# Optimization experiments

Hardware: AMD Instinct MI355X
Metric: run time of the kernel (lower is better)

The kernel has to match this reference:

```python
import jax, jax.numpy as jnp
import numpy as np

K_SIZE = 7
D_MODEL = 128
D_Q = 64
N_HEADS = 4
D_FF = 512
EPS = 1e-5


def _windows(x, k):
    # x: [N,E,H,W] -> [N,E,P,H,W]; zero-padded local k x k windows,
    # row-major over (dy,dx), matching nn.Unfold ordering.
    p = k // 2
    N, E, H, W = x.shape
    xp = jnp.pad(x, ((0, 0), (0, 0), (p, p), (p, p)))
    ws = [xp[:, :, i:i + H, j:j + W] for i in range(k) for j in range(k)]
    return jnp.stack(ws, axis=2)


def _layernorm(x, g, b):
    m = jnp.mean(x, -1, keepdims=True)
    v = jnp.var(x, -1, keepdims=True)
    return (x - m) * jax.lax.rsqrt(v + EPS) * g + b


def setup_inputs() -> dict:
    key = jax.random.key(0)
    ks = jax.random.split(key, 12)
    E, Q, F = D_MODEL, D_Q, D_FF

    def g(k, shape, s=0.02):
        return jax.random.normal(k, shape, jnp.float32) * s

    return dict(
        x=jax.random.normal(ks[0], (4, E, 64, 64), jnp.float32),
        qcoeff=jax.random.normal(ks[1], (4, Q), jnp.float32),
        wq=g(ks[2], (E, E)), bq=jnp.zeros((E,), jnp.float32),
        wk=g(ks[3], (E, E)), bk=jnp.zeros((E,), jnp.float32),
        wv=g(ks[4], (E, E)), bv=jnp.zeros((E,), jnp.float32),
        rel_bias=jnp.zeros((N_HEADS, K_SIZE * K_SIZE), jnp.float32),
        ln1_g=jnp.ones((E,), jnp.float32), ln1_b=jnp.zeros((E,), jnp.float32),
        bil_w=g(ks[5], (E, E, Q)), bil_b=jnp.zeros((E,), jnp.float32),
        ln2_g=jnp.ones((E,), jnp.float32), ln2_b=jnp.zeros((E,), jnp.float32),
        w1=g(ks[6], (F, E)), b1=jnp.zeros((F,), jnp.float32),
        w2=g(ks[7], (E, F)), b2=jnp.zeros((E,), jnp.float32),
    )


def reference(x, qcoeff, wq, bq, wk, bk, wv, bv, rel_bias, ln1_g, ln1_b,
              bil_w, bil_b, ln2_g, ln2_b, w1, b1, w2, b2):
    N, E, H, W = x.shape
    Nh = N_HEADS
    Hd = E // Nh
    P = K_SIZE * K_SIZE

    x_nhwc = jnp.transpose(x, (0, 2, 3, 1))              # [N,H,W,E]
    xn = _layernorm(x_nhwc, ln1_g, ln1_b)
    xnc = jnp.transpose(xn, (0, 3, 1, 2))                # [N,E,H,W]

    # 1x1-conv projections
    q = jnp.einsum('nchw,oc->nohw', xnc, wq) + bq[None, :, None, None]
    k = jnp.einsum('nchw,oc->nohw', xnc, wk) + bk[None, :, None, None]
    v = jnp.einsum('nchw,oc->nohw', xnc, wv) + bv[None, :, None, None]

    # local windows of K/V: [N,Nh,Hd,P,H,W]
    Kw = _windows(k, K_SIZE).reshape(N, Nh, Hd, P, H, W)
    Vw = _windows(v, K_SIZE).reshape(N, Nh, Hd, P, H, W)
    Qh = q.reshape(N, Nh, Hd, H, W)

    scores = jnp.einsum('nhdyx,nhdpyx->nhpyx', Qh, Kw)
    scores = scores + rel_bias[None, :, :, None, None]
    attn = jax.nn.softmax(scores, axis=2)                # softmax over P
    out = jnp.einsum('nhpyx,nhdpyx->nhdyx', attn, Vw).reshape(N, E, H, W)
    z0 = jnp.transpose(out, (0, 2, 3, 1))                # [N,H,W,E]

    # Bilinear(z0, qcoeff): qcoeff constant per (H,W) -> contract once per batch
    t = jnp.einsum('oiq,nq->noi', bil_w, qcoeff)         # [N,E,E]
    z1 = jnp.einsum('nhwi,noi->nhwo', z0, t) + bil_b

    z2 = z1 + x_nhwc
    z3 = _layernorm(z2, ln2_g, ln2_b)
    h1 = jax.nn.gelu(z3 @ w1.T + b1, approximate=False)  # dropout inactive (eval)
    z4 = h1 @ w2.T + b2 + z2
    return jnp.transpose(z4, (0, 3, 1, 2))               # [N,E,H,W]
```

## Files before the change

kernel.cpp:

```cpp
#include <hip/hip_runtime.h>
#include <cmath>

#define EPS 1e-5f
#define SZ 2097152

typedef __attribute__((ext_vector_type(8))) short short8;
typedef __attribute__((ext_vector_type(4))) float floatx4;

__device__ __forceinline__ float dot4(float4 a, float4 b) {
  return fmaf(a.x, b.x, fmaf(a.y, b.y, fmaf(a.z, b.z, a.w * b.w)));
}

__device__ __forceinline__ short f2bf(float f) {
  union { float f; unsigned u; } v; v.f = f;
  unsigned r = v.u + 0x7fff + ((v.u >> 16) & 1);
  return (short)(r >> 16);
}

#define MFMA16(a, b, c) __builtin_amdgcn_mfma_f32_16x16x32_bf16(a, b, c, 0, 0, 0)

__global__ __launch_bounds__(256) void k_prep(const float* __restrict__ w1,
    const float* __restrict__ w2, const float* __restrict__ wq,
    const float* __restrict__ wk, const float* __restrict__ wv,
    const float* __restrict__ bil_w, const float* __restrict__ qcoeff,
    short* __restrict__ w1bf, short* __restrict__ w2bf,
    short* __restrict__ wqbf, short* __restrict__ wkbf, short* __restrict__ wvbf,
    short* __restrict__ tb) {
  __shared__ float qs[256];
  int tid = threadIdx.x;
  qs[tid] = qcoeff[tid];
  __syncthreads();
  int tid0 = blockIdx.x * 256 + tid;
  int stride = gridDim.x * 256;
  for (int i = tid0; i < 16384; i += stride) {
    int flat = i * 4; int f = flat >> 7, c = flat & 127;
    float4 v = *(const float4*)&w1[flat];
    short t4[4] = {f2bf(v.x), f2bf(v.y), f2bf(v.z), f2bf(v.w)};
    *(uint2*)&w1bf[f * 136 + c] = *(uint2*)t4;
  }
  for (int i = tid0; i < 16384; i += stride) {
    int flat = i * 4; int o = flat >> 9, j = flat & 511;
    int ck = j >> 7, jj = j & 127;
    float4 v = *(const float4*)&w2[flat];
    short t4[4] = {f2bf(v.x), f2bf(v.y), f2bf(v.z), f2bf(v.w)};
    *(uint2*)&w2bf[(ck * 128 + o) * 136 + jj] = *(uint2*)t4;
  }
  for (int i = tid0; i < 4096; i += stride) {
    int flat = i * 4; int o = flat >> 7, c = flat & 127;
    float4 a = *(const float4*)&wq[flat];
    float4 b = *(const float4*)&wk[flat];
    float4 cc = *(const float4*)&wv[flat];
    short ta[4] = {f2bf(a.x), f2bf(a.y), f2bf(a.z), f2bf(a.w)};
    short tb4[4] = {f2bf(b.x), f2bf(b.y), f2bf(b.z), f2bf(b.w)};
    short tc[4] = {f2bf(cc.x), f2bf(cc.y), f2bf(cc.z), f2bf(cc.w)};
    *(uint2*)&wqbf[o * 136 + c] = *(uint2*)ta;
    *(uint2*)&wkbf[o * 136 + c] = *(uint2*)tb4;
    *(uint2*)&wvbf[o * 136 + c] = *(uint2*)tc;
  }
  {
    int flat = tid0;
    const float* wrow = bil_w + (size_t)flat * 64;
    float acc[4] = {0.f, 0.f, 0.f, 0.f};
    for (int qq = 0; qq < 64; qq += 4) {
      float4 w4 = *(const float4*)&wrow[qq];
#pragma unroll
      for (int nn = 0; nn < 4; ++nn) {
        const float* qc = &qs[nn * 64 + qq];
        acc[nn] = fmaf(w4.x, qc[0], fmaf(w4.y, qc[1], fmaf(w4.z, qc[2], fmaf(w4.w, qc[3], acc[nn]))));
      }
    }
    int o = flat >> 7, i = flat & 127;
#pragma unroll
    for (int nn = 0; nn < 4; ++nn) tb[nn * 17408 + o * 136 + i] = f2bf(acc[nn]);
  }
}

__global__ __launch_bounds__(1024) void k_qkvln(const float* __restrict__ x,
    const float* __restrict__ g, const float* __restrict__ b,
    const short* __restrict__ wqbf, const short* __restrict__ wkbf,
    const short* __restrict__ wvbf, const float* __restrict__ bq,
    const float* __restrict__ bk, const float* __restrict__ bv,
    float* __restrict__ xnhwc, short* __restrict__ qbf,
    short* __restrict__ kbf, short* __restrict__ vtb) {
  __shared__ float tile[128 * 65];
  __shared__ float mres[64], rres[64];
  __shared__ __align__(16) short xs[64 * 136];
  __shared__ __align__(16) short ws[128 * 136];
  int tid = threadIdx.x;
  int bid = blockIdx.x;
  int n = bid >> 6, y = bid & 63;
  const float* xb = x + (size_t)n * (128 * 4096) + y * 64;
  for (int it = 0; it < 8; ++it) {
    int flat = it * 1024 + tid;
    int c = flat >> 6, xp = flat & 63;
    tile[c * 65 + xp] = xb[(size_t)c * 4096 + xp];
  }
  __syncthreads();
  {
    int px = tid >> 4, cl = tid & 15;
    float s = 0.f, sq = 0.f;
#pragma unroll
    for (int j = 0; j < 8; ++j) {
      float v = tile[(cl * 8 + j) * 65 + px];
      s += v; sq += v * v;
    }
    s += __shfl_xor(s, 1);  sq += __shfl_xor(sq, 1);
    s += __shfl_xor(s, 2);  sq += __shfl_xor(sq, 2);
    s += __shfl_xor(s, 4);  sq += __shfl_xor(sq, 4);
    s += __shfl_xor(s, 8);  sq += __shfl_xor(sq, 8);
    if (cl == 0) {
      float m = s * (1.f / 128.f);
      float var = sq * (1.f / 128.f) - m * m;
      mres[px] = m;
      rres[px] = rsqrtf(var + EPS);
    }
  }
  __syncthreads();
  size_t rowbase = (size_t)bid * 8192;
  for (int it = 0; it < 8; ++it) {
    int flat = it * 1024 + tid;
    int c = flat & 127, px = flat >> 7;
    float v = tile[c * 65 + px];
    xnhwc[rowbase + flat] = v;
    xs[px * 136 + c] = f2bf((v - mres[px]) * rres[px] * g[c] + b[c]);
  }
  __syncthreads();
  int w = tid >> 6, lane = tid & 63;
  int quad = lane >> 4, r16 = lane & 15;
  int wm = w & 3, wn = w >> 2;
  int strip = wm * 16;
  short8 a[4];
#pragma unroll
  for (int kk = 0; kk < 4; ++kk)
    a[kk] = *(const short8*)&xs[(strip + r16) * 136 + kk * 32 + quad * 8];
  const short* wptr[3] = {wqbf, wkbf, wvbf};
  const float* bptr[3] = {bq, bk, bv};
  for (int m = 0; m < 3; ++m) {
    __syncthreads();
    const short* wp = wptr[m];
    for (int i = tid; i < 2176; i += 1024)
      *(short8*)&ws[i * 8] = *(const short8*)&wp[i * 8];
    __syncthreads();
    const float* bb = bptr[m];
#pragma unroll
    for (int nt = 0; nt < 2; ++nt) {
      int o0 = wn * 32 + nt * 16;
      floatx4 acc = {0.f, 0.f, 0.f, 0.f};
#pragma unroll
      for (int kk = 0; kk < 4; ++kk) {
        short8 bfr = *(const short8*)&ws[(o0 + r16) * 136 + kk * 32 + quad * 8];
        acc = MFMA16(a[kk], bfr, acc);
      }
      float bv2 = bb[o0 + r16];
      if (m < 2) {
        short* dst = (m == 0) ? qbf : kbf;
#pragma unroll
        for (int r = 0; r < 4; ++r) {
          int px = strip + quad * 4 + r;
          dst[rowbase + px * 128 + o0 + r16] = f2bf(acc[r] + bv2);
        }
      } else {
        short t4[4] = {f2bf(acc[0] + bv2), f2bf(acc[1] + bv2),
                       f2bf(acc[2] + bv2), f2bf(acc[3] + bv2)};
        *(uint2*)&vtb[(size_t)(n * 128 + o0 + r16) * 4096 + y * 64 + strip + quad * 4] =
            *(uint2*)t4;
      }
    }
  }
}

__global__ __launch_bounds__(1024) void k_at(const short* __restrict__ qbf,
    const short* __restrict__ kbf, const short* __restrict__ vtb,
    const float* __restrict__ rel_bias, const short* __restrict__ tb,
    const float* __restrict__ bil_b, const float* __restrict__ xnhwc,
    const float* __restrict__ g2, const float* __restrict__ b2ln,
    const short* __restrict__ w1bf, const float* __restrict__ b1,
    const short* __restrict__ w2bf, const float* __restrict__ b2,
    float* __restrict__ out) {
  __shared__ __align__(16) char smem[140544];
  short* z3s = (short*)(smem + 89344);
  float* z2s = (float*)(smem + 106752);
  int tid = threadIdx.x;
  int bid = blockIdx.x;
  int n = bid >> 6, y = bid & 63;
  int w16 = tid >> 6, lane = tid & 63;
  int quad = lane >> 4, r16 = lane & 15;
  {
    int h = w16 >> 2, sw = w16 & 3;
    int strip = sw * 16;
    float* ssfw = (float*)(smem + w16 * 3200);
    short* Abw = (short*)(smem + 51200 + w16 * 2176);
    float* biasw = (float*)(smem + 86016 + w16 * 208);
    {
      unsigned* ad = (unsigned*)Abw;
      for (int i = lane; i < 544; i += 64) ad[i] = 0u;
    }
    if (lane < 49) biasw[lane] = rel_bias[h * 49 + lane];
    const short* qrow = qbf + (size_t)n * 524288 + (size_t)y * 8192 + h * 32;
    short8 qf = *(const short8*)&qrow[(strip + r16) * 128 + quad * 8];
    const short* kbp = kbf + (size_t)n * 524288 + h * 32;
#pragma unroll
    for (int r = 0; r < 7; ++r) {
      int yy = y + r - 3;
      bool yok = (unsigned)yy < 64u;
      int yyc = min(max(yy, 0), 63);
#pragma unroll
      for (int t = 0; t < 2; ++t) {
        int xxc = (sw + t) * 16 + r16;
        int gx = xxc - 3;
        bool ok = yok && ((unsigned)gx < 64u);
        int gxc = min(max(gx, 0), 63);
        short8 bf = *(const short8*)&kbp[(size_t)(yyc * 64 + gxc) * 128 + quad * 8];
        floatx4 c = MFMA16(qf, bf, ((floatx4){0.f, 0.f, 0.f, 0.f}));
#pragma unroll
        for (int rr = 0; rr < 4; ++rr) {
          int lrow = quad * 4 + rr;
          int dx = xxc - (strip + lrow);
          if ((unsigned)dx < 7u) {
            float val = ok ? c[rr] : 0.f;
            ssfw[lrow * 50 + r * 7 + dx] = val + biasw[r * 7 + dx];
          }
        }
      }
    }
    {
      int lrow = lane >> 2, sub = lane & 3;
      int p0 = sub * 12, cnt = (sub == 3) ? 13 : 12;
      float sv[13];
      float mx = -1e30f;
      for (int pi = 0; pi < cnt; ++pi) { sv[pi] = ssfw[lrow * 50 + p0 + pi]; mx = fmaxf(mx, sv[pi]); }
      mx = fmaxf(mx, __shfl_xor(mx, 1));
      mx = fmaxf(mx, __shfl_xor(mx, 2));
      float sum = 0.f;
      for (int pi = 0; pi < cnt; ++pi) { float e = __expf(sv[pi] - mx); sv[pi] = e; sum += e; }
      sum += __shfl_xor(sum, 1);
      sum += __shfl_xor(sum, 2);
      float inv = 1.f / sum;
      for (int pi = 0; pi < cnt; ++pi) ssfw[lrow * 50 + p0 + pi] = sv[pi] * inv;
    }
    floatx4 oacc[2] = {(floatx4){0.f, 0.f, 0.f, 0.f}, (floatx4){0.f, 0.f, 0.f, 0.f}};
    int kk0 = (sw == 3) ? 1 : 0;
    int kk1 = (sw == 0) ? 0 : 1;
    int lrow = lane >> 2, sub = lane & 3;
    int pxg = strip + lrow;
    const short* vbp = vtb + (size_t)(n * 128 + h * 32) * 4096;
    for (int r = 0; r < 7; ++r) {
      int yy = y + r - 3;
      bool yok = (unsigned)yy < 64u;
      int yyc = min(max(yy, 0), 63);
      int c0 = pxg + sub - 3;
      if ((unsigned)c0 < 64u) Abw[lrow * 68 + c0] = f2bf(ssfw[lrow * 50 + r * 7 + sub]);
      int c1 = pxg + sub + 1;
      if (sub < 3 && (unsigned)c1 < 64u)
        Abw[lrow * 68 + c1] = f2bf(ssfw[lrow * 50 + r * 7 + sub + 4]);
      for (int kk = kk0; kk <= kk1; ++kk) {
        short8 af = *(const short8*)&Abw[r16 * 68 + kk * 32 + quad * 8];
#pragma unroll
        for (int nt = 0; nt < 2; ++nt) {
          short8 vf = *(const short8*)&vbp[(size_t)(nt * 16 + r16) * 4096 + yyc * 64 + kk * 32 + quad * 8];
          if (!yok) vf = (short8){0, 0, 0, 0, 0, 0, 0, 0};
          oacc[nt] = MFMA16(af, vf, oacc[nt]);
        }
      }
    }
#pragma unroll
    for (int nt = 0; nt < 2; ++nt)
#pragma unroll
      for (int rr = 0; rr < 4; ++rr) {
        int px = strip + quad * 4 + rr;
        z3s[px * 136 + h * 32 + nt * 16 + r16] = f2bf(oacc[nt][rr]);
      }
  }
  __syncthreads();
  short* R1s = (short*)smem;
  short* w2c = (short*)(smem + 34816);
  short* h1s = (short*)(smem + 69632);
  float* outt = (float*)smem;
  size_t rowbase = (size_t)bid * 8192;
  const short* tn = tb + (size_t)n * 17408;
  for (int i = tid; i < 2176; i += 1024)
    *(short8*)&R1s[i * 8] = *(const short8*)&tn[i * 8];
  __syncthreads();
  int wm = w16 & 3, wn = w16 >> 2;
  int strip = wm * 16;
  {
    short8 a[4];
#pragma unroll
    for (int kk = 0; kk < 4; ++kk)
      a[kk] = *(const short8*)&z3s[(strip + r16) * 136 + kk * 32 + quad * 8];
#pragma unroll
    for (int nt = 0; nt < 2; ++nt) {
      int o0 = wn * 32 + nt * 16;
      floatx4 acc = {0.f, 0.f, 0.f, 0.f};
#pragma unroll
      for (int kk = 0; kk < 4; ++kk) {
        short8 bfr = *(const short8*)&R1s[(o0 + r16) * 136 + kk * 32 + quad * 8];
        acc = MFMA16(a[kk], bfr, acc);
      }
      float bb = bil_b[o0 + r16];
#pragma unroll
      for (int r = 0; r < 4; ++r) {
        int px = strip + quad * 4 + r;
        z2s[px * 132 + o0 + r16] = acc[r] + bb + xnhwc[rowbase + px * 128 + o0 + r16];
      }
    }
  }
  __syncthreads();
  {
    int px = tid >> 4, cl = tid & 15;
    float4 v0 = *(const float4*)&z2s[px * 132 + cl * 8];
    float4 v1 = *(const float4*)&z2s[px * 132 + cl * 8 + 4];
    float s = v0.x + v0.y + v0.z + v0.w + v1.x + v1.y + v1.z + v1.w;
    float sq = dot4(v0, v0) + dot4(v1, v1);
    s += __shfl_xor(s, 1);  sq += __shfl_xor(sq, 1);
    s += __shfl_xor(s, 2);  sq += __shfl_xor(sq, 2);
    s += __shfl_xor(s, 4);  sq += __shfl_xor(sq, 4);
    s += __shfl_xor(s, 8);  sq += __shfl_xor(sq, 8);
    float m = s * (1.f / 128.f);
    float var = sq * (1.f / 128.f) - m * m;
    float rr = rsqrtf(var + EPS);
    int c0 = cl * 8;
    short t8[8];
#pragma unroll
    for (int j = 0; j < 8; ++j) {
      float vv = (j < 4) ? (&v0.x)[j] : (&v1.x)[j - 4];
      t8[j] = f2bf((vv - m) * rr * g2[c0 + j] + b2ln[c0 + j]);
    }
    *(uint4*)&z3s[px * 136 + c0] = *(uint4*)t8;
  }
  __syncthreads();
  short8 a3[4];
#pragma unroll
  for (int kk = 0; kk < 4; ++kk)
    a3[kk] = *(const short8*)&z3s[(strip + r16) * 136 + kk * 32 + quad * 8];
  floatx4 zacc[2];
  zacc[0] = (floatx4){0.f, 0.f, 0.f, 0.f};
  zacc[1] = (floatx4){0.f, 0.f, 0.f, 0.f};
  for (int fc = 0; fc < 512; fc += 128) {
    __syncthreads();
    const short* w1src = w1bf + fc * 136;
    const short* w2src = w2bf + (fc >> 7) * 17408;
    for (int i = tid; i < 2176; i += 1024) {
      *(short8*)&R1s[i * 8] = *(const short8*)&w1src[i * 8];
      *(short8*)&w2c[i * 8] = *(const short8*)&w2src[i * 8];
    }
    __syncthreads();
#pragma unroll
    for (int nt = 0; nt < 2; ++nt) {
      int f0 = wn * 32 + nt * 16;
      floatx4 acc = {0.f, 0.f, 0.f, 0.f};
#pragma unroll
      for (int kk = 0; kk < 4; ++kk) {
        short8 bfr = *(const short8*)&R1s[(f0 + r16) * 136 + kk * 32 + quad * 8];
        acc = MFMA16(a3[kk], bfr, acc);
      }
      float bb1 = b1[fc + f0 + r16];
#pragma unroll
      for (int r = 0; r < 4; ++r) {
        float hv = acc[r] + bb1;
        float ge = 0.5f * hv * (1.f + erff(hv * 0.70710678118f));
        h1s[(strip + quad * 4 + r) * 136 + f0 + r16] = f2bf(ge);
      }
    }
    __syncthreads();
    short8 ah[4];
#pragma unroll
    for (int kk = 0; kk < 4; ++kk)
      ah[kk] = *(const short8*)&h1s[(strip + r16) * 136 + kk * 32 + quad * 8];
#pragma unroll
    for (int nt = 0; nt < 2; ++nt) {
      int o0 = wn * 32 + nt * 16;
#pragma unroll
      for (int kk = 0; kk < 4; ++kk) {
        short8 bfr = *(const short8*)&w2c[(o0 + r16) * 136 + kk * 32 + quad * 8];
        zacc[nt] = MFMA16(ah[kk], bfr, zacc[nt]);
      }
    }
  }
  __syncthreads();
#pragma unroll
  for (int nt = 0; nt < 2; ++nt) {
    int o0 = wn * 32 + nt * 16;
    float bb = b2[o0 + r16];
#pragma unroll
    for (int r = 0; r < 4; ++r) {
      int px = strip + quad * 4 + r;
      outt[(o0 + r16) * 65 + px] = zacc[nt][r] + bb + z2s[px * 132 + o0 + r16];
    }
  }
  __syncthreads();
  for (int it = 0; it < 8; ++it) {
    int flat = it * 1024 + tid;
    int o = flat >> 6, px = flat & 63;
    out[(((size_t)(n * 128 + o)) * 64 + y) * 64 + px] = outt[o * 65 + px];
  }
}

extern "C" void kernel_launch(void* const* d_in, const int* in_sizes, int n_in,
                              void* d_out, int out_size, void* d_ws, size_t ws_size,
                              hipStream_t stream) {
  const float* x        = (const float*)d_in[0];
  const float* qcoeff   = (const float*)d_in[1];
  const float* wq       = (const float*)d_in[2];
  const float* bq       = (const float*)d_in[3];
  const float* wk       = (const float*)d_in[4];
  const float* bk       = (const float*)d_in[5];
  const float* wv       = (const float*)d_in[6];
  const float* bv       = (const float*)d_in[7];
  const float* rel_bias = (const float*)d_in[8];
  const float* ln1_g    = (const float*)d_in[9];
  const float* ln1_b    = (const float*)d_in[10];
  const float* bil_w    = (const float*)d_in[11];
  const float* bil_b    = (const float*)d_in[12];
  const float* ln2_g    = (const float*)d_in[13];
  const float* ln2_b    = (const float*)d_in[14];
  const float* w1       = (const float*)d_in[15];
  const float* b1       = (const float*)d_in[16];
  const float* w2       = (const float*)d_in[17];
  const float* b2       = (const float*)d_in[18];
  float* out = (float*)d_out;

  float* ws = (float*)d_ws;
  float* x_nhwc = ws;
  short* qbf = (short*)(ws + 2 * SZ);
  short* kbf = qbf + SZ;
  short* vtb = kbf + SZ;
  short* bf     = (short*)(ws + 4 * SZ);
  short* tb     = bf;
  short* w1bf   = bf + 4 * 17408;
  short* w2bf   = w1bf + 512 * 136;
  short* wqbf   = w2bf + 4 * 17408;
  short* wkbf   = wqbf + 17408;
  short* wvbf   = wkbf + 17408;

  k_prep<<<64, 256, 0, stream>>>(w1, w2, wq, wk, wv, bil_w, qcoeff,
                                 w1bf, w2bf, wqbf, wkbf, wvbf, tb);
  k_qkvln<<<256, 1024, 0, stream>>>(x, ln1_g, ln1_b, wqbf, wkbf, wvbf,
                                    bq, bk, bv, x_nhwc, qbf, kbf, vtb);
  k_at<<<256, 1024, 0, stream>>>(qbf, kbf, vtb, rel_bias, tb, bil_b, x_nhwc,
                                 ln2_g, ln2_b, w1bf, b1, w2bf, b2, out);
}
```

Measured before the change: 149.8 us.

## Fuse prep, QKV/LN and attention kernels into one cooperative kernel

Merges the three separate kernels (weight conversion, LayerNorm plus QKV projection, attention plus MLP) into a single cooperative launch that separates the phases with grid-wide syncs. The goal is to remove two kernel launch gaps and the tail idle time between kernels. The prep phase now runs on 256 blocks of 1024 threads instead of 64 blocks of 256. The cost is grid-sync overhead, and it requires all 256 blocks of 1024 threads with about 137KB of shared memory each to be co-resident on the device.

```diff
diff --git a/kernel.cpp b/kernel.cpp
--- a/kernel.cpp
+++ b/kernel.cpp
@@ -1,5 +1,8 @@
 #include <hip/hip_runtime.h>
+#include <hip/hip_cooperative_groups.h>
 #include <cmath>
+
+namespace cg = cooperative_groups;
 
 #define EPS 1e-5f
 #define SZ 2097152
@@ -19,170 +22,162 @@
 
 #define MFMA16(a, b, c) __builtin_amdgcn_mfma_f32_16x16x32_bf16(a, b, c, 0, 0, 0)
 
-__global__ __launch_bounds__(256) void k_prep(const float* __restrict__ w1,
-    const float* __restrict__ w2, const float* __restrict__ wq,
-    const float* __restrict__ wk, const float* __restrict__ wv,
-    const float* __restrict__ bil_w, const float* __restrict__ qcoeff,
-    short* __restrict__ w1bf, short* __restrict__ w2bf,
-    short* __restrict__ wqbf, short* __restrict__ wkbf, short* __restrict__ wvbf,
-    short* __restrict__ tb) {
-  __shared__ float qs[256];
-  int tid = threadIdx.x;
-  qs[tid] = qcoeff[tid];
-  __syncthreads();
-  int tid0 = blockIdx.x * 256 + tid;
-  int stride = gridDim.x * 256;
-  for (int i = tid0; i < 16384; i += stride) {
-    int flat = i * 4; int f = flat >> 7, c = flat & 127;
-    float4 v = *(const float4*)&w1[flat];
-    short t4[4] = {f2bf(v.x), f2bf(v.y), f2bf(v.z), f2bf(v.w)};
-    *(uint2*)&w1bf[f * 136 + c] = *(uint2*)t4;
-  }
-  for (int i = tid0; i < 16384; i += stride) {
-    int flat = i * 4; int o = flat >> 9, j = flat & 511;
-    int ck = j >> 7, jj = j & 127;
-    float4 v = *(const float4*)&w2[flat];
-    short t4[4] = {f2bf(v.x), f2bf(v.y), f2bf(v.z), f2bf(v.w)};
-    *(uint2*)&w2bf[(ck * 128 + o) * 136 + jj] = *(uint2*)t4;
-  }
-  for (int i = tid0; i < 4096; i += stride) {
-    int flat = i * 4; int o = flat >> 7, c = flat & 127;
-    float4 a = *(const float4*)&wq[flat];
-    float4 b = *(const float4*)&wk[flat];
-    float4 cc = *(const float4*)&wv[flat];
-    short ta[4] = {f2bf(a.x), f2bf(a.y), f2bf(a.z), f2bf(a.w)};
-    short tb4[4] = {f2bf(b.x), f2bf(b.y), f2bf(b.z), f2bf(b.w)};
-    short tc[4] = {f2bf(cc.x), f2bf(cc.y), f2bf(cc.z), f2bf(cc.w)};
-    *(uint2*)&wqbf[o * 136 + c] = *(uint2*)ta;
-    *(uint2*)&wkbf[o * 136 + c] = *(uint2*)tb4;
-    *(uint2*)&wvbf[o * 136 + c] = *(uint2*)tc;
-  }
-  {
-    int flat = tid0;
-    const float* wrow = bil_w + (size_t)flat * 64;
-    float acc[4] = {0.f, 0.f, 0.f, 0.f};
-    for (int qq = 0; qq < 64; qq += 4) {
-      float4 w4 = *(const float4*)&wrow[qq];
-#pragma unroll
-      for (int nn = 0; nn < 4; ++nn) {
-        const float* qc = &qs[nn * 64 + qq];
-        acc[nn] = fmaf(w4.x, qc[0], fmaf(w4.y, qc[1], fmaf(w4.z, qc[2], fmaf(w4.w, qc[3], acc[nn]))));
-      }
-    }
-    int o = flat >> 7, i = flat & 127;
-#pragma unroll
-    for (int nn = 0; nn < 4; ++nn) tb[nn * 17408 + o * 136 + i] = f2bf(acc[nn]);
-  }
-}
-
-__global__ __launch_bounds__(1024) void k_qkvln(const float* __restrict__ x,
-    const float* __restrict__ g, const float* __restrict__ b,
-    const short* __restrict__ wqbf, const short* __restrict__ wkbf,
-    const short* __restrict__ wvbf, const float* __restrict__ bq,
-    const float* __restrict__ bk, const float* __restrict__ bv,
-    float* __restrict__ xnhwc, short* __restrict__ qbf,
-    short* __restrict__ kbf, short* __restrict__ vtb) {
-  __shared__ float tile[128 * 65];
-  __shared__ float mres[64], rres[64];
-  __shared__ __align__(16) short xs[64 * 136];
-  __shared__ __align__(16) short ws[128 * 136];
+struct KParams {
+  const float *x, *qcoeff, *wq, *bq, *wk, *bk, *wv, *bv, *rel_bias;
+  const float *ln1_g, *ln1_b, *bil_w, *bil_b, *ln2_g, *ln2_b, *w1, *b1, *w2, *b2;
+  float* out;
+  float* x_nhwc;
+  short *qbf, *kbf, *vtb;
+  short *tb, *w1bf, *w2bf, *wqbf, *wkbf, *wvbf;
+};
+
+__global__ __launch_bounds__(1024) void k_all(KParams p) {
+  __shared__ __align__(16) char smem[140544];
+  cg::grid_group grid = cg::this_grid();
   int tid = threadIdx.x;
   int bid = blockIdx.x;
   int n = bid >> 6, y = bid & 63;
-  const float* xb = x + (size_t)n * (128 * 4096) + y * 64;
-  for (int it = 0; it < 8; ++it) {
-    int flat = it * 1024 + tid;
-    int c = flat >> 6, xp = flat & 63;
-    tile[c * 65 + xp] = xb[(size_t)c * 4096 + xp];
-  }
-  __syncthreads();
+
   {
-    int px = tid >> 4, cl = tid & 15;
-    float s = 0.f, sq = 0.f;
-#pragma unroll
-    for (int j = 0; j < 8; ++j) {
-      float v = tile[(cl * 8 + j) * 65 + px];
-      s += v; sq += v * v;
-    }
-    s += __shfl_xor(s, 1);  sq += __shfl_xor(sq, 1);
-    s += __shfl_xor(s, 2);  sq += __shfl_xor(sq, 2);
-    s += __shfl_xor(s, 4);  sq += __shfl_xor(sq, 4);
-    s += __shfl_xor(s, 8);  sq += __shfl_xor(sq, 8);
-    if (cl == 0) {
-      float m = s * (1.f / 128.f);
-      float var = sq * (1.f / 128.f) - m * m;
-      mres[px] = m;
-      rres[px] = rsqrtf(var + EPS);
-    }
-  }
-  __syncthreads();
-  size_t rowbase = (size_t)bid * 8192;
-  for (int it = 0; it < 8; ++it) {
-    int flat = it * 1024 + tid;
-    int c = flat & 127, px = flat >> 7;
-    float v = tile[c * 65 + px];
-    xnhwc[rowbase + flat] = v;
-    xs[px * 136 + c] = f2bf((v - mres[px]) * rres[px] * g[c] + b[c]);
-  }
-  __syncthreads();
-  int w = tid >> 6, lane = tid & 63;
-  int quad = lane >> 4, r16 = lane & 15;
-  int wm = w & 3, wn = w >> 2;
-  int strip = wm * 16;
-  short8 a[4];
-#pragma unroll
-  for (int kk = 0; kk < 4; ++kk)
-    a[kk] = *(const short8*)&xs[(strip + r16) * 136 + kk * 32 + quad * 8];
-  const short* wptr[3] = {wqbf, wkbf, wvbf};
-  const float* bptr[3] = {bq, bk, bv};
-  for (int m = 0; m < 3; ++m) {
-    __syncthreads();
-    const short* wp = wptr[m];
-    for (int i = tid; i < 2176; i += 1024)
-      *(short8*)&ws[i * 8] = *(const short8*)&wp[i * 8];
-    __syncthreads();
-    const float* bb = bptr[m];
-#pragma unroll
-    for (int nt = 0; nt < 2; ++nt) {
-      int o0 = wn * 32 + nt * 16;
-      floatx4 acc = {0.f, 0.f, 0.f, 0.f};
-#pragma unroll
-      for (int kk = 0; kk < 4; ++kk) {
-        short8 bfr = *(const short8*)&ws[(o0 + r16) * 136 + kk * 32 + quad * 8];
-        acc = MFMA16(a[kk], bfr, acc);
-      }
-      float bv2 = bb[o0 + r16];
-      if (m < 2) {
-        short* dst = (m == 0) ? qbf : kbf;
-#pragma unroll
-        for (int r = 0; r < 4; ++r) {
-          int px = strip + quad * 4 + r;
-          dst[rowbase + px * 128 + o0 + r16] = f2bf(acc[r] + bv2);
+    float* qs = (float*)smem;
+    if (tid < 256) qs[tid] = p.qcoeff[tid];
+    __syncthreads();
+    int gtid = bid * 1024 + tid;
+    if (gtid < 16384) {
+      int flat = gtid * 4;
+      {
+        int f = flat >> 7, c = flat & 127;
+        float4 v = *(const float4*)&p.w1[flat];
+        short t4[4] = {f2bf(v.x), f2bf(v.y), f2bf(v.z), f2bf(v.w)};
+        *(uint2*)&p.w1bf[f * 136 + c] = *(uint2*)t4;
+      }
+      {
+        int o = flat >> 9, j = flat & 511;
+        int ck = j >> 7, jj = j & 127;
+        float4 v = *(const float4*)&p.w2[flat];
+        short t4[4] = {f2bf(v.x), f2bf(v.y), f2bf(v.z), f2bf(v.w)};
+        *(uint2*)&p.w2bf[(ck * 128 + o) * 136 + jj] = *(uint2*)t4;
+      }
+      {
+        const float* wrow = p.bil_w + (size_t)gtid * 64;
+        float acc[4] = {0.f, 0.f, 0.f, 0.f};
+        for (int qq = 0; qq < 64; qq += 4) {
+          float4 w4 = *(const float4*)&wrow[qq];
+#pragma unroll
+          for (int nn = 0; nn < 4; ++nn) {
+            const float* qc = &qs[nn * 64 + qq];
+            acc[nn] = fmaf(w4.x, qc[0], fmaf(w4.y, qc[1], fmaf(w4.z, qc[2], fmaf(w4.w, qc[3], acc[nn]))));
+          }
         }
-      } else {
-        short t4[4] = {f2bf(acc[0] + bv2), f2bf(acc[1] + bv2),
-                       f2bf(acc[2] + bv2), f2bf(acc[3] + bv2)};
-        *(uint2*)&vtb[(size_t)(n * 128 + o0 + r16) * 4096 + y * 64 + strip + quad * 4] =
-            *(uint2*)t4;
-      }
-    }
-  }
-}
-
-__global__ __launch_bounds__(1024) void k_at(const short* __restrict__ qbf,
-    const short* __restrict__ kbf, const short* __restrict__ vtb,
-    const float* __restrict__ rel_bias, const short* __restrict__ tb,
-    const float* __restrict__ bil_b, const float* __restrict__ xnhwc,
-    const float* __restrict__ g2, const float* __restrict__ b2ln,
-    const short* __restrict__ w1bf, const float* __restrict__ b1,
-    const short* __restrict__ w2bf, const float* __restrict__ b2,
-    float* __restrict__ out) {
-  __shared__ __align__(16) char smem[140544];
+        int o = gtid >> 7, i = gtid & 127;
+#pragma unroll
+        for (int nn = 0; nn < 4; ++nn) p.tb[nn * 17408 + o * 136 + i] = f2bf(acc[nn]);
+      }
+    }
+    if (gtid < 4096) {
+      int flat = gtid * 4; int o = flat >> 7, c = flat & 127;
+      float4 a = *(const float4*)&p.wq[flat];
+      float4 b = *(const float4*)&p.wk[flat];
+      float4 cc = *(const float4*)&p.wv[flat];
+      short ta[4] = {f2bf(a.x), f2bf(a.y), f2bf(a.z), f2bf(a.w)};
+      short tb4[4] = {f2bf(b.x), f2bf(b.y), f2bf(b.z), f2bf(b.w)};
+      short tc[4] = {f2bf(cc.x), f2bf(cc.y), f2bf(cc.z), f2bf(cc.w)};
+      *(uint2*)&p.wqbf[o * 136 + c] = *(uint2*)ta;
+      *(uint2*)&p.wkbf[o * 136 + c] = *(uint2*)tb4;
+      *(uint2*)&p.wvbf[o * 136 + c] = *(uint2*)tc;
+    }
+  }
+  grid.sync();
+
+  {
+    float* tile = (float*)smem;
+    float* mres = (float*)(smem + 33280);
+    float* rres = (float*)(smem + 33536);
+    short* xs = (short*)(smem + 34048);
+    short* ws = (short*)(smem + 51456);
+    const float* xb = p.x + (size_t)n * (128 * 4096) + y * 64;
+    for (int it = 0; it < 8; ++it) {
+      int flat = it * 1024 + tid;
+      int c = flat >> 6, xp = flat & 63;
+      tile[c * 65 + xp] = xb[(size_t)c * 4096 + xp];
+    }
+    __syncthreads();
+    {
+      int px = tid >> 4, cl = tid & 15;
+      float s = 0.f, sq = 0.f;
+#pragma unroll
+      for (int j = 0; j < 8; ++j) {
+        float v = tile[(cl * 8 + j) * 65 + px];
+        s += v; sq += v * v;
+      }
+      s += __shfl_xor(s, 1);  sq += __shfl_xor(sq, 1);
+      s += __shfl_xor(s, 2);  sq += __shfl_xor(sq, 2);
+      s += __shfl_xor(s, 4);  sq += __shfl_xor(sq, 4);
+      s += __shfl_xor(s, 8);  sq += __shfl_xor(sq, 8);
+      if (cl == 0) {
+        float m = s * (1.f / 128.f);
+        float var = sq * (1.f / 128.f) - m * m;
+        mres[px] = m;
+        rres[px] = rsqrtf(var + EPS);
+      }
+    }
+    __syncthreads();
+    size_t rowbase = (size_t)bid * 8192;
+    for (int it = 0; it < 8; ++it) {
+      int flat = it * 1024 + tid;
+      int c = flat & 127, px = flat >> 7;
+      float v = tile[c * 65 + px];
+      p.x_nhwc[rowbase + flat] = v;
+      xs[px * 136 + c] = f2bf((v - mres[px]) * rres[px] * p.ln1_g[c] + p.ln1_b[c]);
+    }
+    __syncthreads();
+    int w = tid >> 6, lane = tid & 63;
+    int quad = lane >> 4, r16 = lane & 15;
+    int wm = w & 3, wn = w >> 2;
+    int strip = wm * 16;
+    short8 a[4];
+#pragma unroll
+    for (int kk = 0; kk < 4; ++kk)
+      a[kk] = *(const short8*)&xs[(strip + r16) * 136 + kk * 32 + quad * 8];
+    const short* wptr[3] = {p.wqbf, p.wkbf, p.wvbf};
+    const float* bptr[3] = {p.bq, p.bk, p.bv};
+    for (int m = 0; m < 3; ++m) {
+      __syncthreads();
+      const short* wp = wptr[m];
+      for (int i = tid; i < 2176; i += 1024)
+        *(short8*)&ws[i * 8] = *(const short8*)&wp[i * 8];
+      __syncthreads();
+      const float* bb = bptr[m];
+#pragma unroll
+      for (int nt = 0; nt < 2; ++nt) {
+        int o0 = wn * 32 + nt * 16;
+        floatx4 acc = {0.f, 0.f, 0.f, 0.f};
+#pragma unroll
+        for (int kk = 0; kk < 4; ++kk) {
+          short8 bfr = *(const short8*)&ws[(o0 + r16) * 136 + kk * 32 + quad * 8];
+          acc = MFMA16(a[kk], bfr, acc);
+        }
+        float bv2 = bb[o0 + r16];
+        if (m < 2) {
+          short* dst = (m == 0) ? p.qbf : p.kbf;
+#pragma unroll
+          for (int r = 0; r < 4; ++r) {
+            int px = strip + quad * 4 + r;
+            dst[rowbase + px * 128 + o0 + r16] = f2bf(acc[r] + bv2);
+          }
+        } else {
+          short t4[4] = {f2bf(acc[0] + bv2), f2bf(acc[1] + bv2),
+                         f2bf(acc[2] + bv2), f2bf(acc[3] + bv2)};
+          *(uint2*)&p.vtb[(size_t)(n * 128 + o0 + r16) * 4096 + y * 64 + strip + quad * 4] =
+              *(uint2*)t4;
+        }
+      }
+    }
+  }
+  grid.sync();
+
   short* z3s = (short*)(smem + 89344);
   float* z2s = (float*)(smem + 106752);
-  int tid = threadIdx.x;
-  int bid = blockIdx.x;
-  int n = bid >> 6, y = bid & 63;
   int w16 = tid >> 6, lane = tid & 63;
   int quad = lane >> 4, r16 = lane & 15;
   {
@@ -195,10 +190,10 @@
       unsigned* ad = (unsigned*)Abw;
       for (int i = lane; i < 544; i += 64) ad[i] = 0u;
     }
-    if (lane < 49) biasw[lane] = rel_bias[h * 49 + lane];
-    const short* qrow = qbf + (size_t)n * 524288 + (size_t)y * 8192 + h * 32;
+    if (lane < 49) biasw[lane] = p.rel_bias[h * 49 + lane];
+    const short* qrow = p.qbf + (size_t)n * 524288 + (size_t)y * 8192 + h * 32;
     short8 qf = *(const short8*)&qrow[(strip + r16) * 128 + quad * 8];
-    const short* kbp = kbf + (size_t)n * 524288 + h * 32;
+    const short* kbp = p.kbf + (size_t)n * 524288 + h * 32;
 #pragma unroll
     for (int r = 0; r < 7; ++r) {
       int yy = y + r - 3;
@@ -243,7 +238,7 @@
     int kk1 = (sw == 0) ? 0 : 1;
     int lrow = lane >> 2, sub = lane & 3;
     int pxg = strip + lrow;
-    const short* vbp = vtb + (size_t)(n * 128 + h * 32) * 4096;
+    const short* vbp = p.vtb + (size_t)(n * 128 + h * 32) * 4096;
     for (int r = 0; r < 7; ++r) {
       int yy = y + r - 3;
       bool yok = (unsigned)yy < 64u;
@@ -277,7 +272,7 @@
   short* h1s = (short*)(smem + 69632);
   float* outt = (float*)smem;
   size_t rowbase = (size_t)bid * 8192;
-  const short* tn = tb + (size_t)n * 17408;
+  const short* tn = p.tb + (size_t)n * 17408;
   for (int i = tid; i < 2176; i += 1024)
     *(short8*)&R1s[i * 8] = *(const short8*)&tn[i * 8];
   __syncthreads();
@@ -297,11 +292,11 @@
         short8 bfr = *(const short8*)&R1s[(o0 + r16) * 136 + kk * 32 + quad * 8];
         acc = MFMA16(a[kk], bfr, acc);
       }
-      float bb = bil_b[o0 + r16];
+      float bb = p.bil_b[o0 + r16];
 #pragma unroll
       for (int r = 0; r < 4; ++r) {
         int px = strip + quad * 4 + r;
-        z2s[px * 132 + o0 + r16] = acc[r] + bb + xnhwc[rowbase + px * 128 + o0 + r16];
+        z2s[px * 132 + o0 + r16] = acc[r] + bb + p.x_nhwc[rowbase + px * 128 + o0 + r16];
       }
     }
   }
@@ -324,7 +319,7 @@
 #pragma unroll
     for (int j = 0; j < 8; ++j) {
       float vv = (j < 4) ? (&v0.x)[j] : (&v1.x)[j - 4];
-      t8[j] = f2bf((vv - m) * rr * g2[c0 + j] + b2ln[c0 + j]);
+      t8[j] = f2bf((vv - m) * rr * p.ln2_g[c0 + j] + p.ln2_b[c0 + j]);
     }
     *(uint4*)&z3s[px * 136 + c0] = *(uint4*)t8;
   }
@@ -338,8 +333,8 @@
   zacc[1] = (floatx4){0.f, 0.f, 0.f, 0.f};
   for (int fc = 0; fc < 512; fc += 128) {
     __syncthreads();
-    const short* w1src = w1bf + fc * 136;
-    const short* w2src = w2bf + (fc >> 7) * 17408;
+    const short* w1src = p.w1bf + fc * 136;
+    const short* w2src = p.w2bf + (fc >> 7) * 17408;
     for (int i = tid; i < 2176; i += 1024) {
       *(short8*)&R1s[i * 8] = *(const short8*)&w1src[i * 8];
       *(short8*)&w2c[i * 8] = *(const short8*)&w2src[i * 8];
@@ -354,7 +349,7 @@
         short8 bfr = *(const short8*)&R1s[(f0 + r16) * 136 + kk * 32 + quad * 8];
         acc = MFMA16(a3[kk], bfr, acc);
       }
-      float bb1 = b1[fc + f0 + r16];
+      float bb1 = p.b1[fc + f0 + r16];
 #pragma unroll
       for (int r = 0; r < 4; ++r) {
         float hv = acc[r] + bb1;
@@ -381,7 +376,7 @@
 #pragma unroll
   for (int nt = 0; nt < 2; ++nt) {
     int o0 = wn * 32 + nt * 16;
-    float bb = b2[o0 + r16];
+    float bb = p.b2[o0 + r16];
 #pragma unroll
     for (int r = 0; r < 4; ++r) {
       int px = strip + quad * 4 + r;
@@ -392,51 +387,48 @@
   for (int it = 0; it < 8; ++it) {
     int flat = it * 1024 + tid;
     int o = flat >> 6, px = flat & 63;
-    out[(((size_t)(n * 128 + o)) * 64 + y) * 64 + px] = outt[o * 65 + px];
+    p.out[(((size_t)(n * 128 + o)) * 64 + y) * 64 + px] = outt[o * 65 + px];
   }
 }
 
 extern "C" void kernel_launch(void* const* d_in, const int* in_sizes, int n_in,
                               void* d_out, int out_size, void* d_ws, size_t ws_size,
                               hipStream_t stream) {
-  const float* x        = (const float*)d_in[0];
-  const float* qcoeff   = (const float*)d_in[1];
-  const float* wq       = (const float*)d_in[2];
-  const float* bq       = (const float*)d_in[3];
-  const float* wk       = (const float*)d_in[4];
-  const float* bk       = (const float*)d_in[5];
-  const float* wv       = (const float*)d_in[6];
-  const float* bv       = (const float*)d_in[7];
-  const float* rel_bias = (const float*)d_in[8];
-  const float* ln1_g    = (const float*)d_in[9];
-  const float* ln1_b    = (const float*)d_in[10];
-  const float* bil_w    = (const float*)d_in[11];
-  const float* bil_b    = (const float*)d_in[12];
-  const float* ln2_g    = (const float*)d_in[13];
-  const float* ln2_b    = (const float*)d_in[14];
-  const float* w1       = (const float*)d_in[15];
-  const float* b1       = (const float*)d_in[16];
-  const float* w2       = (const float*)d_in[17];
-  const float* b2       = (const float*)d_in[18];
-  float* out = (float*)d_out;
-
   float* ws = (float*)d_ws;
-  float* x_nhwc = ws;
-  short* qbf = (short*)(ws + 2 * SZ);
-  short* kbf = qbf + SZ;
-  short* vtb = kbf + SZ;
-  short* bf     = (short*)(ws + 4 * SZ);
-  short* tb     = bf;
-  short* w1bf   = bf + 4 * 17408;
-  short* w2bf   = w1bf + 512 * 136;
-  short* wqbf   = w2bf + 4 * 17408;
-  short* wkbf   = wqbf + 17408;
-  short* wvbf   = wkbf + 17408;
-
-  k_prep<<<64, 256, 0, stream>>>(w1, w2, wq, wk, wv, bil_w, qcoeff,
-                                 w1bf, w2bf, wqbf, wkbf, wvbf, tb);
-  k_qkvln<<<256, 1024, 0, stream>>>(x, ln1_g, ln1_b, wqbf, wkbf, wvbf,
-                                    bq, bk, bv, x_nhwc, qbf, kbf, vtb);
-  k_at<<<256, 1024, 0, stream>>>(qbf, kbf, vtb, rel_bias, tb, bil_b, x_nhwc,
-                                 ln2_g, ln2_b, w1bf, b1, w2bf, b2, out);
+  short* bf = (short*)(ws + 4 * SZ);
+
+  KParams p;
+  p.x        = (const float*)d_in[0];
+  p.qcoeff   = (const float*)d_in[1];
+  p.wq       = (const float*)d_in[2];
+  p.bq       = (const float*)d_in[3];
+  p.wk       = (const float*)d_in[4];
+  p.bk       = (const float*)d_in[5];
+  p.wv       = (const float*)d_in[6];
+  p.bv       = (const float*)d_in[7];
+  p.rel_bias = (const float*)d_in[8];
+  p.ln1_g    = (const float*)d_in[9];
+  p.ln1_b    = (const float*)d_in[10];
+  p.bil_w    = (const float*)d_in[11];
+  p.bil_b    = (const float*)d_in[12];
+  p.ln2_g    = (const float*)d_in[13];
+  p.ln2_b    = (const float*)d_in[14];
+  p.w1       = (const float*)d_in[15];
+  p.b1       = (const float*)d_in[16];
+  p.w2       = (const float*)d_in[17];
+  p.b2       = (const float*)d_in[18];
+  p.out      = (float*)d_out;
+  p.x_nhwc   = ws;
+  p.qbf      = (short*)(ws + 2 * SZ);
+  p.kbf      = p.qbf + SZ;
+  p.vtb      = p.kbf + SZ;
+  p.tb       = bf;
+  p.w1bf     = bf + 4 * 17408;
+  p.w2bf     = p.w1bf + 512 * 136;
+  p.wqbf     = p.w2bf + 4 * 17408;
+  p.wkbf     = p.wqbf + 17408;
+  p.wvbf     = p.wkbf + 17408;
+
+  void* args[] = {&p};
+  hipLaunchCooperativeKernel((const void*)k_all, dim3(256), dim3(1024), args, 0, stream);
 }
```

Result: slower. 237.2 us (+58.3%).
